# Kernel tuning notes

Measured on AMD Instinct MI355X. Metric: run time of the kernel, lower is better.

The kernel has to match this reference:

```python
import jax, jax.numpy as jnp
import numpy as np

WS = (4, 4, 4)          # window size per axis
DISP = (2, 2, 2)        # cyclic-shift displacement = window_size // 2
HEADS = 8
HEAD_DIM = 32
DIM = 256


def _make_mask(x_shift, y_shift, z_shift):
    wx, wy, wz = WS
    dx, dy, dz = DISP
    m = np.zeros((wx, wy, wz, wx, wy, wz), np.float32)
    if x_shift:
        m[-dx:, :, :, :-dx, :, :] = -np.inf
        m[:-dx, :, :, -dx:, :, :] = -np.inf
    if y_shift:
        m[:, -dy:, :, :, :-dy, :] = -np.inf
        m[:, :-dy, :, :, -dy:, :] = -np.inf
    if z_shift:
        m[:, :, -dz:, :, :, :-dz] = -np.inf
        m[:, :, :-dz, :, :, -dz:] = -np.inf
    W = wx * wy * wz
    return jnp.asarray(m.reshape(W, W))


def setup_inputs() -> dict:
    key = jax.random.key(0)
    k1, k2, k3 = jax.random.split(key, 3)
    inner = HEADS * HEAD_DIM
    x = jax.random.normal(k1, (1, 48, 48, 48, DIM), jnp.float32)
    w_qkv = jax.random.normal(k2, (DIM, 3 * inner), jnp.float32) * (DIM ** -0.5)
    w_out = jax.random.normal(k3, (inner, DIM), jnp.float32) * (inner ** -0.5)
    b_out = jnp.zeros((DIM,), jnp.float32)
    return {"x": x, "w_qkv": w_qkv, "w_out": w_out, "b_out": b_out}


def reference(x, w_qkv, w_out, b_out):
    wx, wy, wz = WS
    h, d = HEADS, HEAD_DIM
    scale = d ** -0.5
    xm = _make_mask(True, False, False)
    ym = _make_mask(False, True, False)
    zm = _make_mask(False, False, True)

    # cyclic shift
    x = jnp.roll(x, (-DISP[0], -DISP[1], -DISP[2]), axis=(1, 2, 3))
    b, nx, ny, nz, _ = x.shape
    nwx, nwy, nwz = nx // wx, ny // wy, nz // wz
    W = wx * wy * wz
    nw = nwx * nwy * nwz

    qkv = x @ w_qkv                      # [b,nx,ny,nz,3*h*d]
    q, k, v = jnp.split(qkv, 3, axis=-1)

    def win(t):
        t = t.reshape(b, nwx, wx, nwy, wy, nwz, wz, h, d)
        t = t.transpose(0, 7, 1, 3, 5, 2, 4, 6, 8)   # b h nwx nwy nwz wx wy wz d
        return t.reshape(b, h, nw, W, d)

    q, k, v = win(q), win(k), win(v)
    dots = jnp.einsum('bhwid,bhwjd->bhwij', q, k) * scale

    # additive shift masks on the last window along each axis
    dots = dots.reshape(b, h, nwx, nwy, nwz, W, W)
    dots = dots.at[:, :, -1, :, :].add(xm)
    dots = dots.at[:, :, :, -1, :].add(ym)
    dots = dots.at[:, :, :, :, -1].add(zm)
    # faithful replication of original einops label mismatch: the tensor is
    # (nwx,nwy,nwz) but is flattened as if labeled (n_y,n_z,n_x) -> (n_x n_y n_z),
    # i.e. actual flatten order (nwz, nwx, nwy)
    dots = dots.transpose(0, 1, 4, 2, 3, 5, 6).reshape(b, h, nw, W, W)

    attn = jax.nn.softmax(dots, axis=-1)
    out = jnp.einsum('bhwij,bhwjd->bhwid', attn, v)

    out = out.reshape(b, h, nwx, nwy, nwz, wx, wy, wz, d)
    out = out.transpose(0, 2, 5, 3, 6, 4, 7, 1, 8).reshape(b, nx, ny, nz, h * d)
    out = out @ w_out + b_out
    # cyclic back shift
    return jnp.roll(out, DISP, axis=(1, 2, 3))
```

## Files before the change

kernel.cpp:

```cpp
#include <hip/hip_runtime.h>
#include <hip/hip_bf16.h>

typedef __attribute__((ext_vector_type(8))) short short8;
typedef __attribute__((ext_vector_type(4))) float f32x4;

#define NT 110592

static __device__ __forceinline__ unsigned int f2bf(float f){
  unsigned int x; __builtin_memcpy(&x,&f,4);
  x += 0x7fffu + ((x>>16)&1u);
  return x >> 16;
}

static __device__ __forceinline__ void gll16(const unsigned short* g, unsigned short* l){
  typedef const __attribute__((address_space(1))) unsigned int gu32;
  typedef __attribute__((address_space(3))) unsigned int lu32;
  __builtin_amdgcn_global_load_lds((gu32*)(const void*)g, (lu32*)(void*)l, 16, 0, 0);
}

__global__ void prep(const float* __restrict__ x,      unsigned short* __restrict__ xbf,
                     const float* __restrict__ wqkv,   unsigned short* __restrict__ wqkvT,
                     const float* __restrict__ wout,   unsigned short* __restrict__ woutT){
  const int bid = blockIdx.x;
  if (bid < 13824){
    size_t i = ((size_t)bid*256 + threadIdx.x) * 8;
    float4 a = *(const float4*)(x+i), b = *(const float4*)(x+i+4);
    uint4 pk;
    pk.x = f2bf(a.x)|(f2bf(a.y)<<16); pk.y = f2bf(a.z)|(f2bf(a.w)<<16);
    pk.z = f2bf(b.x)|(f2bf(b.y)<<16); pk.w = f2bf(b.z)|(f2bf(b.w)<<16);
    *(uint4*)(xbf+i) = pk;
  } else if (bid < 14592){
    int id = (bid-13824)*256 + threadIdx.x;
    int r = id / 768, c = id - r*768;
    wqkvT[c*256 + r] = (unsigned short)f2bf(wqkv[id]);
  } else {
    int id = (bid-14592)*256 + threadIdx.x;
    int r = id >> 8, c = id & 255;
    woutT[c*256 + r] = (unsigned short)f2bf(wout[id]);
  }
}

template<bool CF32>
__global__ __launch_bounds__(512, 8) void gemm_bt(
    const unsigned short* __restrict__ A,
    const unsigned short* __restrict__ Bt,
    const float* __restrict__ bias,
    void* __restrict__ Cv,
    int M, int N, int K)
{
  __shared__ __align__(16) unsigned short As[2*4096];
  __shared__ __align__(16) unsigned short Bs[2*4096];

  const int nwg = gridDim.x;
  const int bid = blockIdx.x;
  const int qq = nwg >> 3, rr = nwg & 7;
  const int xcd = bid & 7, loc = bid >> 3;
  const int swz = (xcd < rr ? xcd*(qq+1) : rr*(qq+1) + (xcd-rr)*qq) + loc;
  const int nbn = N >> 7;
  const int bn = swz % nbn;
  const int bm = swz / nbn;

  const int tid  = threadIdx.x;
  const int lane = tid & 63;
  const int wave = tid >> 6;
  const int wm = wave >> 1, wn = wave & 1;
  const int l16 = lane & 15, q = lane >> 4;

  const size_t arow0 = (size_t)(bm*128 + (tid>>2))*K;
  const size_t brow0 = (size_t)(bn*128 + (tid>>2))*K;
  const int g8  = ((tid&3) ^ ((tid>>3)&3)) * 8;
  const int cg8 = (q ^ ((l16>>1)&3)) * 8;

  f32x4 acc[2][4] = {};

  for (int k0 = 0; k0 < K; k0 += 64){
    __syncthreads();
    gll16(A  + arow0 + k0 + g8,       &As[tid*8]);
    gll16(A  + arow0 + k0 + 32 + g8,  &As[4096 + tid*8]);
    gll16(Bt + brow0 + k0 + g8,       &Bs[tid*8]);
    gll16(Bt + brow0 + k0 + 32 + g8,  &Bs[4096 + tid*8]);
    __syncthreads();

    #pragma unroll
    for (int h = 0; h < 2; ++h){
      short8 af[2], bfm[4];
      #pragma unroll
      for (int t = 0; t < 2; ++t)
        af[t]  = *(const short8*)&As[h*4096 + (wm*32 + t*16 + l16)*32 + cg8];
      #pragma unroll
      for (int t = 0; t < 4; ++t)
        bfm[t] = *(const short8*)&Bs[h*4096 + (wn*64 + t*16 + l16)*32 + cg8];
      #pragma unroll
      for (int im = 0; im < 2; ++im)
        #pragma unroll
        for (int in = 0; in < 4; ++in)
          acc[im][in] = __builtin_amdgcn_mfma_f32_16x16x32_bf16(af[im], bfm[in], acc[im][in], 0, 0, 0);
    }
  }

  #pragma unroll
  for (int in = 0; in < 4; ++in){
    int col = bn*128 + wn*64 + in*16 + l16;
    float bv = CF32 ? bias[col] : 0.f;
    #pragma unroll
    for (int im = 0; im < 2; ++im){
      int row0 = bm*128 + wm*32 + im*16 + q*4;
      #pragma unroll
      for (int r = 0; r < 4; ++r){
        if (CF32) ((float*)Cv)[(size_t)(row0 + r)*N + col] = acc[im][in][r] + bv;
        else ((unsigned short*)Cv)[(size_t)(row0 + r)*N + col] = (unsigned short)f2bf(acc[im][in][r]);
      }
    }
  }
}

__global__ __launch_bounds__(128) void attn3d(
    const unsigned short* __restrict__ qkv,
    unsigned short* __restrict__ aout)
{
  __shared__ __align__(16) unsigned short sh[2*6912];
  const int tid  = threadIdx.x;
  const int wave = tid >> 6, lane = tid & 63;
  const int l16  = lane & 15, q = lane >> 4;
  unsigned short* P  = sh + wave*6912;
  unsigned short* VT = P + 64*72;

  const int wh   = blockIdx.x*2 + wave;
  const int head = wh & 7;
  const int w    = wh >> 3;
  const int A  = w / 144;
  const int B  = (w / 12) % 12;
  const int Cw = w % 12;

  const int iyy = l16 >> 2, izz = l16 & 3;
  int tok_qk[4], tok_v[4];
  #pragma unroll
  for (int t = 0; t < 4; ++t){
    int px = (4*B  + t   + 2) % 48;
    int py = (4*Cw + iyy + 2) % 48;
    int pz = (4*A  + izz + 2) % 48;
    tok_qk[t] = (px*48 + py)*48 + pz;
    int vx = (4*A  + t   + 2) % 48;
    int vy = (4*B  + iyy + 2) % 48;
    int vz = (4*Cw + izz + 2) % 48;
    tok_v[t] = (vx*48 + vy)*48 + vz;
  }

  {
    int sx = (4*A  + (lane>>4)     + 2) % 48;
    int sy = (4*B  + ((lane>>2)&3) + 2) % 48;
    int sz = (4*Cw + (lane&3)      + 2) % 48;
    const unsigned short* vp = qkv + (size_t)((sx*48+sy)*48+sz)*768 + 512 + head*32;
    uint4 v0 = *(const uint4*)(vp);
    uint4 v1 = *(const uint4*)(vp+8);
    uint4 v2 = *(const uint4*)(vp+16);
    uint4 v3 = *(const uint4*)(vp+24);
    unsigned vv[16] = {v0.x,v0.y,v0.z,v0.w, v1.x,v1.y,v1.z,v1.w,
                       v2.x,v2.y,v2.z,v2.w, v3.x,v3.y,v3.z,v3.w};
    #pragma unroll
    for (int u = 0; u < 16; ++u){
      VT[(2*u+0)*72 + lane] = (unsigned short)(vv[u] & 0xffffu);
      VT[(2*u+1)*72 + lane] = (unsigned short)(vv[u] >> 16);
    }
  }

  short8 kf[4], qf[4];
  #pragma unroll
  for (int t = 0; t < 4; ++t){
    const unsigned short* base = qkv + (size_t)tok_qk[t]*768 + head*32 + q*8;
    qf[t] = *(const short8*)(base);
    kf[t] = *(const short8*)(base + 256);
  }

  f32x4 s[4][4] = {};
  __builtin_amdgcn_s_setprio(1);
  #pragma unroll
  for (int im = 0; im < 4; ++im)
    #pragma unroll
    for (int jn = 0; jn < 4; ++jn)
      s[im][jn] = __builtin_amdgcn_mfma_f32_16x16x32_bf16(kf[im], qf[jn], s[im][jn], 0, 0, 0);
  __builtin_amdgcn_s_setprio(0);

  const float scale = 0.17677669529663687f;
  const int mx = (B == 11), my = (Cw == 11), mz = (A == 11);
  const int dy = my & ((q>>1) ^ (l16>>3));
  float sum4[4] = {0.f,0.f,0.f,0.f};
  #pragma unroll
  for (int jn = 0; jn < 4; ++jn){
    #pragma unroll
    for (int im = 0; im < 4; ++im){
      const int dxy = (mx & ((im>>1) ^ (jn>>1))) | dy;
      float e0 = (dxy | (mz & (0 ^ ((l16>>1)&1)))) ? 0.f : __expf(s[im][jn][0]*scale);
      float e1 = (dxy | (mz & (0 ^ ((l16>>1)&1)))) ? 0.f : __expf(s[im][jn][1]*scale);
      float e2 = (dxy | (mz & (1 ^ ((l16>>1)&1)))) ? 0.f : __expf(s[im][jn][2]*scale);
      float e3 = (dxy | (mz & (1 ^ ((l16>>1)&1)))) ? 0.f : __expf(s[im][jn][3]*scale);
      sum4[jn] += (e0+e1)+(e2+e3);
      uint2 pk;
      pk.x = f2bf(e0) | (f2bf(e1)<<16);
      pk.y = f2bf(e2) | (f2bf(e3)<<16);
      *(uint2*)&P[(jn*16+l16)*72 + im*16 + q*4] = pk;
    }
  }
  #pragma unroll
  for (int jn = 0; jn < 4; ++jn){
    float sj = sum4[jn];
    sj += __shfl_xor(sj, 16);
    sj += __shfl_xor(sj, 32);
    sum4[jn] = 1.f / sj;
  }

  f32x4 o[2][4] = {};
  __builtin_amdgcn_s_setprio(1);
  #pragma unroll
  for (int ks = 0; ks < 2; ++ks){
    short8 vf[2], pf[4];
    #pragma unroll
    for (int dt = 0; dt < 2; ++dt)
      vf[dt] = *(const short8*)&VT[(dt*16 + l16)*72 + ks*32 + q*8];
    #pragma unroll
    for (int it = 0; it < 4; ++it)
      pf[it] = *(const short8*)&P[(it*16 + l16)*72 + ks*32 + q*8];
    #pragma unroll
    for (int dt = 0; dt < 2; ++dt)
      #pragma unroll
      for (int it = 0; it < 4; ++it)
        o[dt][it] = __builtin_amdgcn_mfma_f32_16x16x32_bf16(vf[dt], pf[it], o[dt][it], 0, 0, 0);
  }
  __builtin_amdgcn_s_setprio(0);

  #pragma unroll
  for (int it = 0; it < 4; ++it){
    float inv = sum4[it];
    unsigned short* op = aout + (size_t)tok_v[it]*256 + head*32;
    #pragma unroll
    for (int dt = 0; dt < 2; ++dt){
      uint2 pk;
      pk.x = f2bf(o[dt][it][0]*inv) | (f2bf(o[dt][it][1]*inv) << 16);
      pk.y = f2bf(o[dt][it][2]*inv) | (f2bf(o[dt][it][3]*inv) << 16);
      *(uint2*)(op + dt*16 + q*4) = pk;
    }
  }
}

extern "C" void kernel_launch(void* const* d_in, const int* in_sizes, int n_in,
                              void* d_out, int out_size, void* d_ws, size_t ws_size,
                              hipStream_t stream) {
  const float* x     = (const float*)d_in[0];
  const float* w_qkv = (const float*)d_in[1];
  const float* w_out = (const float*)d_in[2];
  const float* b_out = (const float*)d_in[3];
  float* out = (float*)d_out;

  unsigned short* qkv   = (unsigned short*)d_ws;
  unsigned short* xbf   = qkv   + (size_t)NT*768;
  unsigned short* aout  = xbf;
  unsigned short* wqkvT = xbf   + (size_t)NT*256;
  unsigned short* woutT = wqkvT + (size_t)768*256;

  prep<<<dim3(14848), dim3(256), 0, stream>>>(x, xbf, w_qkv, wqkvT, w_out, woutT);

  gemm_bt<false><<<dim3((768/128)*(NT/128)), dim3(512), 0, stream>>>(xbf, wqkvT, nullptr, qkv, NT, 768, 256);

  attn3d<<<dim3(13824/2), dim3(128), 0, stream>>>(qkv, aout);

  gemm_bt<true><<<dim3((256/128)*(NT/128)), dim3(512), 0, stream>>>(aout, woutT, b_out, out, NT, 256, 256);
}
```

Baseline: 339.4 us.

## Software-pipeline GEMM K loop with a four-slab LDS ring buffer

The bf16 GEMM main loop changes from a sync, load, sync, compute pattern over 64-wide K chunks to a fully unrolled loop over eight 32-wide slabs. It uses a four-buffer LDS ring with two slabs of global-to-LDS prefetch in flight, managed by explicit vmcnt waits and a single barrier per slab. The goal is to hide global load latency behind MFMA work and to drop the double barrier. In exchange LDS per block doubles, the occupancy hint drops from 8 to 4, and K is now hardcoded to 256.

```diff
diff --git a/kernel.cpp b/kernel.cpp
--- a/kernel.cpp
+++ b/kernel.cpp
@@ -41,15 +41,15 @@
 }
 
 template<bool CF32>
-__global__ __launch_bounds__(512, 8) void gemm_bt(
+__global__ __launch_bounds__(512, 4) void gemm_bt(
     const unsigned short* __restrict__ A,
     const unsigned short* __restrict__ Bt,
     const float* __restrict__ bias,
     void* __restrict__ Cv,
     int M, int N, int K)
 {
-  __shared__ __align__(16) unsigned short As[2*4096];
-  __shared__ __align__(16) unsigned short Bs[2*4096];
+  __shared__ __align__(16) unsigned short As[4*4096];
+  __shared__ __align__(16) unsigned short Bs[4*4096];
 
   const int nwg = gridDim.x;
   const int bid = blockIdx.x;
@@ -73,29 +73,37 @@
 
   f32x4 acc[2][4] = {};
 
-  for (int k0 = 0; k0 < K; k0 += 64){
-    __syncthreads();
-    gll16(A  + arow0 + k0 + g8,       &As[tid*8]);
-    gll16(A  + arow0 + k0 + 32 + g8,  &As[4096 + tid*8]);
-    gll16(Bt + brow0 + k0 + g8,       &Bs[tid*8]);
-    gll16(Bt + brow0 + k0 + 32 + g8,  &Bs[4096 + tid*8]);
-    __syncthreads();
-
-    #pragma unroll
-    for (int h = 0; h < 2; ++h){
-      short8 af[2], bfm[4];
+  auto stage = [&](int slab){
+    const int b = slab & 3;
+    gll16(A  + arow0 + slab*32 + g8, &As[b*4096 + tid*8]);
+    gll16(Bt + brow0 + slab*32 + g8, &Bs[b*4096 + tid*8]);
+  };
+
+  stage(0);
+  stage(1);
+
+  #pragma unroll
+  for (int t = 0; t < 8; ++t){
+    if (t < 6) stage(t + 2);
+    if (t < 6)       asm volatile("s_waitcnt vmcnt(4)" ::: "memory");
+    else if (t == 6) asm volatile("s_waitcnt vmcnt(2)" ::: "memory");
+    else             asm volatile("s_waitcnt vmcnt(0)" ::: "memory");
+    __builtin_amdgcn_s_barrier();
+    __builtin_amdgcn_sched_barrier(0);
+
+    const int b = t & 3;
+    short8 af[2], bfm[4];
+    #pragma unroll
+    for (int tt = 0; tt < 2; ++tt)
+      af[tt]  = *(const short8*)&As[b*4096 + (wm*32 + tt*16 + l16)*32 + cg8];
+    #pragma unroll
+    for (int tt = 0; tt < 4; ++tt)
+      bfm[tt] = *(const short8*)&Bs[b*4096 + (wn*64 + tt*16 + l16)*32 + cg8];
+    #pragma unroll
+    for (int im = 0; im < 2; ++im)
       #pragma unroll
-      for (int t = 0; t < 2; ++t)
-        af[t]  = *(const short8*)&As[h*4096 + (wm*32 + t*16 + l16)*32 + cg8];
-      #pragma unroll
-      for (int t = 0; t < 4; ++t)
-        bfm[t] = *(const short8*)&Bs[h*4096 + (wn*64 + t*16 + l16)*32 + cg8];
-      #pragma unroll
-      for (int im = 0; im < 2; ++im)
-        #pragma unroll
-        for (int in = 0; in < 4; ++in)
-          acc[im][in] = __builtin_amdgcn_mfma_f32_16x16x32_bf16(af[im], bfm[in], acc[im][in], 0, 0, 0);
-    }
+      for (int in = 0; in < 4; ++in)
+        acc[im][in] = __builtin_amdgcn_mfma_f32_16x16x32_bf16(af[im], bfm[in], acc[im][in], 0, 0, 0);
   }
 
   #pragma unroll
```

Result: slower. 360.2 us (+6.1%).
